# Kernel tuning notes

Hardware: AMD Instinct MI355X
Metric: run time of the kernel (lower is better)

Reference implementation:

```python
import jax, jax.numpy as jnp
import numpy as np

DIM = 128
SEQ = 8192

def setup_inputs() -> dict:
    key = jax.random.key(0)
    kq, kk, kv = jax.random.split(key, 3)
    Q = jax.random.normal(kq, (SEQ, DIM), dtype=jnp.float32)
    K = jax.random.normal(kk, (SEQ, DIM), dtype=jnp.float32)
    V = jax.random.normal(kv, (SEQ, DIM), dtype=jnp.float32)
    return {"Q": Q, "K": K, "V": V}

def reference(Q, K, V):
    # scores: [SEQ, SEQ]; scaled by sqrt(embedding dim) as in the torch module
    scale = 1.0 / np.sqrt(DIM).astype(np.float32)
    scores = jnp.einsum('qd,kd->qk', Q, K) * scale
    attn = jax.nn.softmax(scores, axis=-1)
    z = jnp.einsum('qk,kd->qd', attn, V)
    return z
```

## Files before the change

kernel.cpp:

```cpp
#include <hip/hip_runtime.h>
#include <hip/hip_bf16.h>

#define DIM 128
#define SEQ 8192
#define NSPLIT 8
#define SPLITLEN (SEQ / NSPLIT)
#define NT64 (SPLITLEN / 64)
#define SCALE_L2E 0.1275325340249306f
#define PSTR 72

#define OPB_BYTES ((size_t)NSPLIT * SEQ * DIM * 2)
#define LP_BYTE   OPB_BYTES
#define KST_BYTE  (LP_BYTE + (size_t)NSPLIT * SEQ * 4)
#define VST_BYTE  (KST_BYTE + (size_t)SEQ * DIM * 2)
#define WS_NEED   (VST_BYTE + (size_t)SEQ * DIM * 2)

typedef __attribute__((ext_vector_type(8))) short short8;
typedef __attribute__((ext_vector_type(4))) float f32x4;
typedef __attribute__((ext_vector_type(16))) float f32x16;

__device__ __forceinline__ unsigned short f2bf(float f) {
  return __builtin_bit_cast(unsigned short, __float2bfloat16(f));
}
__device__ __forceinline__ unsigned int f2bf2(float a, float b) {
  return (unsigned int)f2bf(a) | ((unsigned int)f2bf(b) << 16);
}
__device__ __forceinline__ float bf2f(unsigned short u) {
  return __builtin_bit_cast(float, (unsigned int)u << 16);
}
__device__ __forceinline__ float fast_exp2(float x) {
#if __has_builtin(__builtin_amdgcn_exp2f)
  return __builtin_amdgcn_exp2f(x);
#else
  return exp2f(x);
#endif
}
__device__ __forceinline__ void async_cp16(const void* g, void* l) {
  __builtin_amdgcn_global_load_lds(
      (const __attribute__((address_space(1))) void*)g,
      (__attribute__((address_space(3))) void*)l, 16, 0, 0);
}

__global__ __launch_bounds__(256) void prep_kv(
    const float* __restrict__ K, const float* __restrict__ V,
    unsigned short* __restrict__ Kst, unsigned short* __restrict__ Vst) {
  const int t = threadIdx.x;
  if (blockIdx.x < 256) {
    __shared__ __align__(16) unsigned short klds[32 * 128];
    const int r0 = blockIdx.x * 32;
    #pragma unroll
    for (int i = 0; i < 4; i++) {
      int idx = i * 256 + t;
      int r  = idx >> 5;
      int c4 = (idx & 31) << 2;
      int g  = c4 >> 3;
      const float4 f = *(const float4*)(K + (size_t)(r0 + r) * DIM + c4);
      uint2 u = {f2bf2(f.x, f.y), f2bf2(f.z, f.w)};
      *(uint2*)&klds[r * 128 + ((g ^ (r & 7)) << 3) + (c4 & 7)] = u;
    }
    __syncthreads();
    const size_t base = (size_t)blockIdx.x * 512;
    #pragma unroll
    for (int e = 0; e < 2; e++) {
      int c  = e * 256 + t;
      int n  = c & 31;
      int hi = (c >> 5) & 1;
      int cc = c >> 6;
      int g  = cc * 2 + hi;
      uint4 u = *(const uint4*)&klds[n * 128 + ((g ^ (n & 7)) << 3)];
      *(uint4*)&Kst[(base + (size_t)g * 32 + n) * 8] = u;
    }
  } else {
    int c    = (blockIdx.x - 256) * 256 + t;
    int n    = c & 31;
    int hi   = (c >> 5) & 1;
    int c2   = (c >> 6) & 3;
    int dt   = (c >> 8) & 3;
    int tile = c >> 10;
    const float* src = V + (size_t)(tile * 64 + c2 * 16 + hi * 8) * DIM + dt * 32 + n;
    float v[8];
    #pragma unroll
    for (int j = 0; j < 8; j++) v[j] = src[(size_t)j * DIM];
    uint4 u;
    u.x = f2bf2(v[0], v[1]); u.y = f2bf2(v[2], v[3]);
    u.z = f2bf2(v[4], v[5]); u.w = f2bf2(v[6], v[7]);
    size_t oc = ((((size_t)(tile * 2 + (c2 >> 1)) * 4 + dt) * 2 + (c2 & 1)) * 2 + hi) * 32 + n;
    *(uint4*)&Vst[oc * 8] = u;
  }
}

__global__ __launch_bounds__(256, 2) void attn_main(
    const float* __restrict__ Q, const unsigned short* __restrict__ Kst,
    const unsigned short* __restrict__ Vst,
    unsigned short* __restrict__ opb, float* __restrict__ lp) {
  __shared__ __align__(16) unsigned short kt[8192];
  __shared__ __align__(16) unsigned short vt[8192];
  __shared__ __align__(16) unsigned short pt[4][32 * PSTR];

  const int tid  = threadIdx.x;
  const int wave = tid >> 6;
  const int lane = tid & 63;
  const int m    = lane & 31;
  const int hi   = lane >> 5;

  const int split = blockIdx.x;
  const int qtile = blockIdx.y;
  const int qbase = qtile * 128 + wave * 32;

  short8 qf[8];
  {
    const float* qrow = Q + (size_t)(qbase + m) * DIM + hi * 8;
    #pragma unroll
    for (int cc = 0; cc < 8; cc++) {
      float4 a = *(const float4*)(qrow + cc * 16);
      float4 b = *(const float4*)(qrow + cc * 16 + 4);
      short8 v;
      unsigned int u0 = f2bf2(a.x * SCALE_L2E, a.y * SCALE_L2E);
      unsigned int u1 = f2bf2(a.z * SCALE_L2E, a.w * SCALE_L2E);
      unsigned int u2 = f2bf2(b.x * SCALE_L2E, b.y * SCALE_L2E);
      unsigned int u3 = f2bf2(b.z * SCALE_L2E, b.w * SCALE_L2E);
      v[0] = (short)(u0 & 0xffff); v[1] = (short)(u0 >> 16);
      v[2] = (short)(u1 & 0xffff); v[3] = (short)(u1 >> 16);
      v[4] = (short)(u2 & 0xffff); v[5] = (short)(u2 >> 16);
      v[6] = (short)(u3 & 0xffff); v[7] = (short)(u3 >> 16);
      qf[cc] = v;
    }
  }

  float lsum[16];
  f32x16 accO[4];
  #pragma unroll
  for (int r = 0; r < 16; r++) lsum[r] = 0.f;
  #pragma unroll
  for (int dt = 0; dt < 4; dt++)
    #pragma unroll
    for (int r = 0; r < 16; r++) accO[dt][r] = 0.f;

  unsigned short* ptw = &pt[wave][0];
  const int tbase32 = split * (SPLITLEN / 32);

  for (int it = 0; it < NT64; it++) {
    const unsigned short* ks = Kst + (size_t)(tbase32 + it * 2) * 4096;
    const unsigned short* vs = Vst + (size_t)(tbase32 + it * 2) * 4096;
    __syncthreads();
    #pragma unroll
    for (int i = 0; i < 4; i++) {
      int ch = wave * 4 + i;
      async_cp16(ks + ch * 512 + lane * 8, (char*)kt + ch * 1024);
      async_cp16(vs + ch * 512 + lane * 8, (char*)vt + ch * 1024);
    }
    __syncthreads();

    f32x16 accS[2];
    #pragma unroll
    for (int kt2 = 0; kt2 < 2; kt2++) {
      f32x16 acc;
      #pragma unroll
      for (int r = 0; r < 16; r++) acc[r] = 0.f;
      #pragma unroll
      for (int cc = 0; cc < 8; cc++) {
        short8 b = *(const short8*)&kt[kt2 * 4096 + ((cc * 2 + hi) * 32 + m) * 8];
        acc = __builtin_amdgcn_mfma_f32_32x32x16_bf16(qf[cc], b, acc, 0, 0, 0);
      }
      accS[kt2] = acc;
    }

    #pragma unroll
    for (int kt2 = 0; kt2 < 2; kt2++) {
      #pragma unroll
      for (int reg = 0; reg < 16; reg++) {
        int row = (reg & 3) + 8 * (reg >> 2) + 4 * hi;
        float p = fast_exp2(accS[kt2][reg]);
        lsum[reg] += p;
        ptw[row * PSTR + kt2 * 32 + m] = f2bf(p);
      }
    }

    short8 ap[4];
    #pragma unroll
    for (int g = 0; g < 4; g++)
      ap[g] = *(const short8*)&ptw[m * PSTR + g * 16 + hi * 8];

    #pragma unroll
    for (int dt = 0; dt < 4; dt++) {
      #pragma unroll
      for (int g = 0; g < 4; g++) {
        short8 b = *(const short8*)&vt[(g >> 1) * 4096 +
                                       ((dt * 4 + (g & 1) * 2 + hi) * 32 + m) * 8];
        accO[dt] = __builtin_amdgcn_mfma_f32_32x32x16_bf16(ap[g], b, accO[dt], 0, 0, 0);
      }
    }
  }

  unsigned short* op = opb + (size_t)split * SEQ * DIM;
  float* lps = lp + (size_t)split * SEQ;
  #pragma unroll
  for (int reg = 0; reg < 16; reg++) {
    float l = lsum[reg];
    l += __shfl_xor(l, 1);
    l += __shfl_xor(l, 2);
    l += __shfl_xor(l, 4);
    l += __shfl_xor(l, 8);
    l += __shfl_xor(l, 16);
    int qrow = qbase + (reg & 3) + 8 * (reg >> 2) + 4 * hi;
    #pragma unroll
    for (int dt = 0; dt < 4; dt++)
      op[(size_t)qrow * DIM + dt * 32 + m] = f2bf(accO[dt][reg]);
    if (m == 0) lps[qrow] = l;
  }
}

__global__ __launch_bounds__(256) void attn_combine(
    const unsigned short* __restrict__ opb, const float* __restrict__ lp,
    float* __restrict__ O) {
  int t = blockIdx.x * 256 + threadIdx.x;
  int qrow = t >> 5;
  int c4   = (t & 31) << 2;
  float denom = 0.f;
  #pragma unroll
  for (int s = 0; s < NSPLIT; s++) denom += lp[(size_t)s * SEQ + qrow];
  float4 acc = {0.f, 0.f, 0.f, 0.f};
  #pragma unroll
  for (int s = 0; s < NSPLIT; s++) {
    ushort4 u = *(const ushort4*)&opb[((size_t)s * SEQ + qrow) * DIM + c4];
    acc.x += bf2f(u.x); acc.y += bf2f(u.y);
    acc.z += bf2f(u.z); acc.w += bf2f(u.w);
  }
  float inv = 1.f / denom;
  float4 out = {acc.x * inv, acc.y * inv, acc.z * inv, acc.w * inv};
  *(float4*)&O[(size_t)qrow * DIM + c4] = out;
}

#define KSTR 136
#define VSTR 72
#define FPSTR 72
__global__ __launch_bounds__(256, 1) void attn_fwd_fb(
    const float* __restrict__ Q, const float* __restrict__ K,
    const float* __restrict__ V, float* __restrict__ O) {
  __shared__ __align__(16) unsigned short kt[64 * KSTR];
  __shared__ __align__(16) unsigned short vt[DIM * VSTR];
  __shared__ __align__(16) unsigned short pt[4][16 * FPSTR];
  const int tid = threadIdx.x, wave = tid >> 6, lane = tid & 63;
  const int l15 = lane & 15, quad = lane >> 4;
  const int qbase = blockIdx.x * 64 + wave * 16;
  short8 qf[4];
  {
    const float* qrow = Q + (size_t)(qbase + l15) * DIM + quad * 8;
    #pragma unroll
    for (int c = 0; c < 4; c++) {
      short8 v;
      #pragma unroll
      for (int j = 0; j < 8; j++) v[j] = (short)f2bf(qrow[c * 32 + j]);
      qf[c] = v;
    }
  }
  float lsum[4] = {0.f, 0.f, 0.f, 0.f};
  f32x4 o[8];
  const f32x4 fzero = {0.f, 0.f, 0.f, 0.f};
  #pragma unroll
  for (int d = 0; d < 8; d++) o[d] = fzero;
  unsigned short* pw = &pt[wave][0];
  for (int kv0 = 0; kv0 < SEQ; kv0 += 64) {
    __syncthreads();
    #pragma unroll
    for (int i = 0; i < 8; i++) {
      int idx = i * 256 + tid;
      int r = idx >> 5, c4 = (idx & 31) << 2;
      const float4 f = *(const float4*)(K + (size_t)(kv0 + r) * DIM + c4);
      uint2 u = {f2bf2(f.x, f.y), f2bf2(f.z, f.w)};
      *(uint2*)&kt[r * KSTR + c4] = u;
    }
    #pragma unroll
    for (int i = 0; i < 8; i++) {
      int idx = i * 256 + tid;
      int c = idx & 127, g = idx >> 7;
      const float* src = V + (size_t)(kv0 + 4 * g) * DIM + c;
      uint2 u = {f2bf2(src[0], src[DIM]), f2bf2(src[2 * DIM], src[3 * DIM])};
      *(uint2*)&vt[c * VSTR + 4 * g] = u;
    }
    __syncthreads();
    f32x4 s[4];
    #pragma unroll
    for (int blk = 0; blk < 4; blk++) {
      f32x4 acc = fzero;
      const unsigned short* kr = &kt[(blk * 16 + l15) * KSTR + quad * 8];
      #pragma unroll
      for (int c = 0; c < 4; c++)
        acc = __builtin_amdgcn_mfma_f32_16x16x32_bf16(qf[c], *(const short8*)&kr[c * 32], acc, 0, 0, 0);
      s[blk] = acc;
    }
    #pragma unroll
    for (int r = 0; r < 4; r++) {
      #pragma unroll
      for (int blk = 0; blk < 4; blk++) {
        float p = fast_exp2(s[blk][r] * SCALE_L2E);
        lsum[r] += p;
        pw[(quad * 4 + r) * FPSTR + blk * 16 + l15] = f2bf(p);
      }
    }
    short8 ap0 = *(const short8*)&pw[l15 * FPSTR + quad * 8];
    short8 ap1 = *(const short8*)&pw[l15 * FPSTR + 32 + quad * 8];
    #pragma unroll
    for (int d = 0; d < 8; d++) {
      const unsigned short* vr = &vt[(d * 16 + l15) * VSTR + quad * 8];
      o[d] = __builtin_amdgcn_mfma_f32_16x16x32_bf16(ap0, *(const short8*)&vr[0], o[d], 0, 0, 0);
      o[d] = __builtin_amdgcn_mfma_f32_16x16x32_bf16(ap1, *(const short8*)&vr[32], o[d], 0, 0, 0);
    }
  }
  #pragma unroll
  for (int r = 0; r < 4; r++) {
    float l = lsum[r];
    l += __shfl_xor(l, 1); l += __shfl_xor(l, 2);
    l += __shfl_xor(l, 4); l += __shfl_xor(l, 8);
    float inv = 1.f / l;
    float* orow = O + (size_t)(qbase + quad * 4 + r) * DIM + l15;
    #pragma unroll
    for (int d = 0; d < 8; d++) orow[d * 16] = o[d][r] * inv;
  }
}

extern "C" void kernel_launch(void* const* d_in, const int* in_sizes, int n_in,
                              void* d_out, int out_size, void* d_ws, size_t ws_size,
                              hipStream_t stream) {
  const float* Q = (const float*)d_in[0];
  const float* K = (const float*)d_in[1];
  const float* V = (const float*)d_in[2];
  float* O = (float*)d_out;
  if (ws_size >= WS_NEED) {
    char* ws = (char*)d_ws;
    unsigned short* opb = (unsigned short*)ws;
    float* lp           = (float*)(ws + LP_BYTE);
    unsigned short* Kst = (unsigned short*)(ws + KST_BYTE);
    unsigned short* Vst = (unsigned short*)(ws + VST_BYTE);
    hipLaunchKernelGGL(prep_kv, dim3(768), dim3(256), 0, stream, K, V, Kst, Vst);
    hipLaunchKernelGGL(attn_main, dim3(NSPLIT, SEQ / 128), dim3(256), 0, stream,
                       Q, Kst, Vst, opb, lp);
    hipLaunchKernelGGL(attn_combine, dim3(1024), dim3(256), 0, stream, opb, lp, O);
  } else {
    hipLaunchKernelGGL(attn_fwd_fb, dim3(SEQ / 64), dim3(256), 0, stream, Q, K, V, O);
  }
}
```

Measured before the change: 115.5 us.

## Fuse K/V prep, split attention and combine into one persistent kernel with grid barriers

Merges the three launches (bf16 K/V restaging, split-K attention, cross-split combine) into a single 512-block kernel that uses two software grid barriers (atomic counter plus spin with s_sleep) between phases. The partial outputs are packed as 64-bit words of four bf16 values and written and read with relaxed agent-scope atomics. This is meant to remove launch overhead and inter-kernel gaps. It relies on all 512 blocks being co-resident, since otherwise the spin barrier deadlocks, and it adds a memset before each launch.

```diff
diff --git a/kernel.cpp b/kernel.cpp
--- a/kernel.cpp
+++ b/kernel.cpp
@@ -6,14 +6,16 @@
 #define NSPLIT 8
 #define SPLITLEN (SEQ / NSPLIT)
 #define NT64 (SPLITLEN / 64)
+#define NBLOCKS 512
 #define SCALE_L2E 0.1275325340249306f
 #define PSTR 72
 
-#define OPB_BYTES ((size_t)NSPLIT * SEQ * DIM * 2)
+#define OPB_BYTES ((size_t)NSPLIT * SEQ * 32 * 8)
 #define LP_BYTE   OPB_BYTES
 #define KST_BYTE  (LP_BYTE + (size_t)NSPLIT * SEQ * 4)
 #define VST_BYTE  (KST_BYTE + (size_t)SEQ * DIM * 2)
-#define WS_NEED   (VST_BYTE + (size_t)SEQ * DIM * 2)
+#define BAR_BYTE  (VST_BYTE + (size_t)SEQ * DIM * 2)
+#define WS_NEED   (BAR_BYTE + 128)
 
 typedef __attribute__((ext_vector_type(8))) short short8;
 typedef __attribute__((ext_vector_type(4))) float f32x4;
@@ -41,58 +43,25 @@
       (__attribute__((address_space(3))) void*)l, 16, 0, 0);
 }
 
-__global__ __launch_bounds__(256) void prep_kv(
-    const float* __restrict__ K, const float* __restrict__ V,
-    unsigned short* __restrict__ Kst, unsigned short* __restrict__ Vst) {
-  const int t = threadIdx.x;
-  if (blockIdx.x < 256) {
-    __shared__ __align__(16) unsigned short klds[32 * 128];
-    const int r0 = blockIdx.x * 32;
-    #pragma unroll
-    for (int i = 0; i < 4; i++) {
-      int idx = i * 256 + t;
-      int r  = idx >> 5;
-      int c4 = (idx & 31) << 2;
-      int g  = c4 >> 3;
-      const float4 f = *(const float4*)(K + (size_t)(r0 + r) * DIM + c4);
-      uint2 u = {f2bf2(f.x, f.y), f2bf2(f.z, f.w)};
-      *(uint2*)&klds[r * 128 + ((g ^ (r & 7)) << 3) + (c4 & 7)] = u;
-    }
-    __syncthreads();
-    const size_t base = (size_t)blockIdx.x * 512;
-    #pragma unroll
-    for (int e = 0; e < 2; e++) {
-      int c  = e * 256 + t;
-      int n  = c & 31;
-      int hi = (c >> 5) & 1;
-      int cc = c >> 6;
-      int g  = cc * 2 + hi;
-      uint4 u = *(const uint4*)&klds[n * 128 + ((g ^ (n & 7)) << 3)];
-      *(uint4*)&Kst[(base + (size_t)g * 32 + n) * 8] = u;
-    }
-  } else {
-    int c    = (blockIdx.x - 256) * 256 + t;
-    int n    = c & 31;
-    int hi   = (c >> 5) & 1;
-    int c2   = (c >> 6) & 3;
-    int dt   = (c >> 8) & 3;
-    int tile = c >> 10;
-    const float* src = V + (size_t)(tile * 64 + c2 * 16 + hi * 8) * DIM + dt * 32 + n;
-    float v[8];
-    #pragma unroll
-    for (int j = 0; j < 8; j++) v[j] = src[(size_t)j * DIM];
-    uint4 u;
-    u.x = f2bf2(v[0], v[1]); u.y = f2bf2(v[2], v[3]);
-    u.z = f2bf2(v[4], v[5]); u.w = f2bf2(v[6], v[7]);
-    size_t oc = ((((size_t)(tile * 2 + (c2 >> 1)) * 4 + dt) * 2 + (c2 & 1)) * 2 + hi) * 32 + n;
-    *(uint4*)&Vst[oc * 8] = u;
-  }
-}
-
-__global__ __launch_bounds__(256, 2) void attn_main(
-    const float* __restrict__ Q, const unsigned short* __restrict__ Kst,
-    const unsigned short* __restrict__ Vst,
-    unsigned short* __restrict__ opb, float* __restrict__ lp) {
+__device__ __forceinline__ void gbar(unsigned int* cnt) {
+  __syncthreads();
+  if (threadIdx.x == 0) {
+    __threadfence();
+    __hip_atomic_fetch_add(cnt, 1u, __ATOMIC_ACQ_REL, __HIP_MEMORY_SCOPE_AGENT);
+    while (__hip_atomic_load(cnt, __ATOMIC_ACQUIRE, __HIP_MEMORY_SCOPE_AGENT) <
+           (unsigned)NBLOCKS) {
+      __builtin_amdgcn_s_sleep(2);
+    }
+  }
+  __syncthreads();
+}
+
+__global__ __launch_bounds__(256, 2) void attn_fused(
+    const float* __restrict__ Q, const float* __restrict__ K,
+    const float* __restrict__ V, unsigned short* __restrict__ Kst,
+    unsigned short* __restrict__ Vst, unsigned long long* __restrict__ opb,
+    float* __restrict__ lp, unsigned int* __restrict__ bar,
+    float* __restrict__ O) {
   __shared__ __align__(16) unsigned short kt[8192];
   __shared__ __align__(16) unsigned short vt[8192];
   __shared__ __align__(16) unsigned short pt[4][32 * PSTR];
@@ -102,9 +71,8 @@
   const int lane = tid & 63;
   const int m    = lane & 31;
   const int hi   = lane >> 5;
-
-  const int split = blockIdx.x;
-  const int qtile = blockIdx.y;
+  const int x = blockIdx.x, y = blockIdx.y;
+  const int split = x, qtile = y;
   const int qbase = qtile * 128 + wave * 32;
 
   short8 qf[8];
@@ -127,6 +95,53 @@
     }
   }
 
+  if (y < 32) {
+    const int t32 = x * 32 + y;
+    const int r0  = t32 * 32;
+    #pragma unroll
+    for (int i = 0; i < 4; i++) {
+      int idx = i * 256 + tid;
+      int r  = idx >> 5;
+      int c4 = (idx & 31) << 2;
+      int g  = c4 >> 3;
+      const float4 f = *(const float4*)(K + (size_t)(r0 + r) * DIM + c4);
+      uint2 u = {f2bf2(f.x, f.y), f2bf2(f.z, f.w)};
+      *(uint2*)&kt[r * 128 + ((g ^ (r & 7)) << 3) + (c4 & 7)] = u;
+    }
+    __syncthreads();
+    const size_t base = (size_t)t32 * 512;
+    #pragma unroll
+    for (int e = 0; e < 2; e++) {
+      int c  = e * 256 + tid;
+      int n  = c & 31;
+      int h2 = (c >> 5) & 1;
+      int cc = c >> 6;
+      int g  = cc * 2 + h2;
+      uint4 u = *(const uint4*)&kt[n * 128 + ((g ^ (n & 7)) << 3)];
+      *(uint4*)&Kst[(base + (size_t)g * 32 + n) * 8] = u;
+    }
+  } else {
+    #pragma unroll
+    for (int e = 0; e < 2; e++) {
+      int c    = x * 16384 + (y - 32) * 512 + e * 256 + tid;
+      int n    = c & 31;
+      int h2   = (c >> 5) & 1;
+      int c2   = (c >> 6) & 3;
+      int dt   = (c >> 8) & 3;
+      int tile = c >> 10;
+      const float* src = V + (size_t)(tile * 64 + c2 * 16 + h2 * 8) * DIM + dt * 32 + n;
+      float v[8];
+      #pragma unroll
+      for (int j = 0; j < 8; j++) v[j] = src[(size_t)j * DIM];
+      uint4 u;
+      u.x = f2bf2(v[0], v[1]); u.y = f2bf2(v[2], v[3]);
+      u.z = f2bf2(v[4], v[5]); u.w = f2bf2(v[6], v[7]);
+      size_t oc = ((((size_t)(tile * 2 + (c2 >> 1)) * 4 + dt) * 2 + (c2 & 1)) * 2 + h2) * 32 + n;
+      *(uint4*)&Vst[oc * 8] = u;
+    }
+  }
+  gbar(&bar[0]);
+
   float lsum[16];
   f32x16 accO[4];
   #pragma unroll
@@ -192,8 +207,6 @@
     }
   }
 
-  unsigned short* op = opb + (size_t)split * SEQ * DIM;
-  float* lps = lp + (size_t)split * SEQ;
   #pragma unroll
   for (int reg = 0; reg < 16; reg++) {
     float l = lsum[reg];
@@ -203,32 +216,47 @@
     l += __shfl_xor(l, 8);
     l += __shfl_xor(l, 16);
     int qrow = qbase + (reg & 3) + 8 * (reg >> 2) + 4 * hi;
-    #pragma unroll
-    for (int dt = 0; dt < 4; dt++)
-      op[(size_t)qrow * DIM + dt * 32 + m] = f2bf(accO[dt][reg]);
-    if (m == 0) lps[qrow] = l;
-  }
-}
-
-__global__ __launch_bounds__(256) void attn_combine(
-    const unsigned short* __restrict__ opb, const float* __restrict__ lp,
-    float* __restrict__ O) {
-  int t = blockIdx.x * 256 + threadIdx.x;
-  int qrow = t >> 5;
-  int c4   = (t & 31) << 2;
-  float denom = 0.f;
-  #pragma unroll
-  for (int s = 0; s < NSPLIT; s++) denom += lp[(size_t)s * SEQ + qrow];
-  float4 acc = {0.f, 0.f, 0.f, 0.f};
-  #pragma unroll
-  for (int s = 0; s < NSPLIT; s++) {
-    ushort4 u = *(const ushort4*)&opb[((size_t)s * SEQ + qrow) * DIM + c4];
-    acc.x += bf2f(u.x); acc.y += bf2f(u.y);
-    acc.z += bf2f(u.z); acc.w += bf2f(u.w);
-  }
-  float inv = 1.f / denom;
-  float4 out = {acc.x * inv, acc.y * inv, acc.z * inv, acc.w * inv};
-  *(float4*)&O[(size_t)qrow * DIM + c4] = out;
+    unsigned long long pk =
+        (unsigned long long)f2bf(accO[0][reg]) |
+        ((unsigned long long)f2bf(accO[1][reg]) << 16) |
+        ((unsigned long long)f2bf(accO[2][reg]) << 32) |
+        ((unsigned long long)f2bf(accO[3][reg]) << 48);
+    __hip_atomic_store(&opb[((size_t)(split * SEQ + qrow) << 5) + m], pk,
+                       __ATOMIC_RELAXED, __HIP_MEMORY_SCOPE_AGENT);
+    if (m == 0)
+      __hip_atomic_store(&lp[(size_t)split * SEQ + qrow], l,
+                         __ATOMIC_RELAXED, __HIP_MEMORY_SCOPE_AGENT);
+  }
+  gbar(&bar[1]);
+
+  {
+    int gid  = (y * 8 + x) * 256 + tid;
+    int qrow = gid >> 4;
+    int w    = gid & 15;
+    float denom = 0.f;
+    float acc[8] = {0.f, 0.f, 0.f, 0.f, 0.f, 0.f, 0.f, 0.f};
+    #pragma unroll
+    for (int s = 0; s < NSPLIT; s++) {
+      denom += __hip_atomic_load(&lp[(size_t)s * SEQ + qrow],
+                                 __ATOMIC_RELAXED, __HIP_MEMORY_SCOPE_AGENT);
+      const size_t rb = ((size_t)(s * SEQ + qrow) << 5);
+      unsigned long long a = __hip_atomic_load(&opb[rb + 2 * w],
+                                 __ATOMIC_RELAXED, __HIP_MEMORY_SCOPE_AGENT);
+      unsigned long long b = __hip_atomic_load(&opb[rb + 2 * w + 1],
+                                 __ATOMIC_RELAXED, __HIP_MEMORY_SCOPE_AGENT);
+      #pragma unroll
+      for (int j = 0; j < 4; j++) {
+        acc[j]     += bf2f((unsigned short)(a >> (16 * j)));
+        acc[4 + j] += bf2f((unsigned short)(b >> (16 * j)));
+      }
+    }
+    float inv = 1.f / denom;
+    #pragma unroll
+    for (int dt = 0; dt < 4; dt++) {
+      float2 o2 = {acc[dt] * inv, acc[4 + dt] * inv};
+      *(float2*)&O[(size_t)qrow * DIM + dt * 32 + 2 * w] = o2;
+    }
+  }
 }
 
 #define KSTR 136
@@ -328,14 +356,14 @@
   float* O = (float*)d_out;
   if (ws_size >= WS_NEED) {
     char* ws = (char*)d_ws;
-    unsigned short* opb = (unsigned short*)ws;
+    unsigned long long* opb = (unsigned long long*)ws;
     float* lp           = (float*)(ws + LP_BYTE);
     unsigned short* Kst = (unsigned short*)(ws + KST_BYTE);
     unsigned short* Vst = (unsigned short*)(ws + VST_BYTE);
-    hipLaunchKernelGGL(prep_kv, dim3(768), dim3(256), 0, stream, K, V, Kst, Vst);
-    hipLaunchKernelGGL(attn_main, dim3(NSPLIT, SEQ / 128), dim3(256), 0, stream,
-                       Q, Kst, Vst, opb, lp);
-    hipLaunchKernelGGL(attn_combine, dim3(1024), dim3(256), 0, stream, opb, lp, O);
+    unsigned int* bar   = (unsigned int*)(ws + BAR_BYTE);
+    hipMemsetAsync(bar, 0, 128, stream);
+    hipLaunchKernelGGL(attn_fused, dim3(8, 64), dim3(256), 0, stream,
+                       Q, K, V, Kst, Vst, opb, lp, bar, O);
   } else {
     hipLaunchKernelGGL(attn_fwd_fb, dim3(SEQ / 64), dim3(256), 0, stream, Q, K, V, O);
   }
```

Result: slower. 215.4 us (+86.5%).
